# Performance work log

Measured on AMD Instinct MI355X. Metric: run time of the kernel, lower is better.

## Reference

```python
import jax, jax.numpy as jnp
import numpy as np

QDEPTH = 8
WIDTH = 64
HEIGHT = 64
WIRES = 12  # ceil(log2(64*64))
BATCH = 1024


def setup_inputs() -> dict:
    key = jax.random.key(0)
    k1, k2 = jax.random.split(key)
    x = jax.random.normal(k1, (BATCH, 1, WIDTH, HEIGHT), dtype=jnp.float32)
    # torch.nn.Parameter(torch.randn(weight_shape) * 0.4)
    weights = jax.random.normal(k2, (QDEPTH, WIRES, 3), dtype=jnp.float32) * 0.4
    return {"x": x, "weights": weights, "reps": 1}


def _rot_matrices(angles):
    # angles: (L, W, 3) -> (L, W, 2, 2) complex64; Rot(phi, theta, omega) = RZ(omega) RY(theta) RZ(phi)
    phi, theta, omega = angles[..., 0], angles[..., 1], angles[..., 2]
    c = jnp.cos(theta * 0.5).astype(jnp.complex64)
    s = jnp.sin(theta * 0.5).astype(jnp.complex64)
    ep = jnp.exp(-0.5j * (phi + omega).astype(jnp.complex64))  # e^{-i(phi+omega)/2}
    em = jnp.exp(-0.5j * (phi - omega).astype(jnp.complex64))  # e^{-i(phi-omega)/2}
    row0 = jnp.stack([ep * c, -jnp.conj(em) * s], axis=-1)
    row1 = jnp.stack([em * s, jnp.conj(ep) * c], axis=-1)
    return jnp.stack([row0, row1], axis=-2)


def _apply_1q(state, U, wire):
    # state: (B, 2, 2, ..., 2); apply 2x2 U on axis wire+1
    ax = wire + 1
    s = jnp.moveaxis(state, ax, -1)
    s = s @ U.T  # out[..., i] = sum_j U[i, j] s[..., j]
    return jnp.moveaxis(s, -1, ax)


def _apply_cnot(state, control, target):
    c, t = control + 1, target + 1
    s0, s1 = jnp.split(state, 2, axis=c)   # control = 0 / 1 halves
    s1 = jnp.flip(s1, axis=t)              # X on target where control = 1
    return jnp.concatenate([s0, s1], axis=c)


def _sel_layer(state, mats_l, r):
    # one StronglyEntanglingLayers layer: Rot on every wire, then CNOT ring of range r
    for w in range(WIRES):
        state = _apply_1q(state, mats_l[w], w)
    for w in range(WIRES):
        state = _apply_cnot(state, w, (w + r) % WIRES)
    return state


def _circuit(state, weights, reps):
    mats = _rot_matrices(jnp.tanh(weights))  # qw_map.tanh applied to raw weights
    for _ in range(reps):
        for l in range(QDEPTH):
            r = (l % (WIRES - 1)) + 1  # PennyLane default ranges
            layer = jax.checkpoint(lambda s, m, _r=r: _sel_layer(s, m, _r))
            state = layer(state, mats[l])
    return state


def reference(x, weights, reps):
    b = x.shape[0]
    v = x.reshape(b, -1)  # (b, 4096)
    norm = jnp.linalg.norm(v, axis=-1, keepdims=True)
    v = (v / norm).astype(jnp.complex64)
    state = v.reshape((b,) + (2,) * WIRES)
    state = _circuit(state, weights, reps)
    out = state.reshape(b, -1) * norm
    return out.reshape(b, 1, WIDTH, HEIGHT)
```

## Files before the change

kernel.cpp:

```cpp
#include <hip/hip_runtime.h>

#define WIRES   12
#define NSTATE  4096
#define QDEPTH  8
#define BLOCK   256
#define PER_T   16

using f2 = __attribute__((ext_vector_type(2))) float;

__device__ __forceinline__ int slotf(int a) { return a + (a >> 4); }

constexpr int colF(int l, int j) {
    int rr = (l % (WIRES - 1)) + 1;
    int v = 1 << j;
    for (int k = WIRES - 1; k >= 0; --k) {
        int bc = 11 - k;
        int bt = 11 - ((k + rr) % WIRES);
        v ^= ((v >> bc) & 1) << bt;
    }
    return v;
}
struct ColsT { int v[QDEPTH][WIRES]; };
constexpr ColsT mkCols() {
    ColsT c{};
    for (int l = 0; l < QDEPTH; ++l)
        for (int j = 0; j < WIRES; ++j) c.v[l][j] = colF(l, j);
    return c;
}
static __device__ const ColsT COLS = mkCols();

__global__ void mats_kernel(const float* __restrict__ wts, f2* __restrict__ mg)
{
    int t = blockIdx.x * blockDim.x + threadIdx.x;
    if (t >= QDEPTH * WIRES) return;
    float phi   = tanhf(wts[t * 3 + 0]);
    float theta = tanhf(wts[t * 3 + 1]);
    float omega = tanhf(wts[t * 3 + 2]);
    float c  = cosf(theta * 0.5f);
    float s  = sinf(theta * 0.5f);
    float a  = 0.5f * (phi + omega);
    float bm = 0.5f * (phi - omega);
    float ca = cosf(a),  sa = sinf(a);
    float cb = cosf(bm), sb = sinf(bm);
    f2* m = mg + t * 8;
    m[0] = f2{ c * ca,  c * ca};
    m[1] = f2{ c * sa, -c * sa};
    m[2] = f2{-s * cb, -s * cb};
    m[3] = f2{ s * sb, -s * sb};
    m[4] = f2{ s * cb,  s * cb};
    m[5] = f2{ s * sb, -s * sb};
    m[6] = f2{ c * ca,  c * ca};
    m[7] = f2{-c * sa,  c * sa};
}

template<int P>
__device__ __forceinline__ void gate(f2 r[PER_T], const f2* __restrict__ m)
{
    const f2 u00r = m[0], u00w = m[1], u01r = m[2], u01w = m[3];
    const f2 u10r = m[4], u10w = m[5], u11r = m[6], u11w = m[7];
    #pragma unroll
    for (int pr = 0; pr < PER_T / 2; pr += 2) {
        const int k0 = ((pr >> P) << (P + 1)) | (pr & ((1 << P) - 1));
        const int k1 = k0 | (1 << P);
        const int q  = pr + 1;
        const int j0 = ((q >> P) << (P + 1)) | (q & ((1 << P) - 1));
        const int j1 = j0 | (1 << P);
        f2 a0, b0, a1, b1;
        asm("v_pk_mul_f32 %0, %4, %8\n\t"
            "v_pk_mul_f32 %1, %4, %12\n\t"
            "v_pk_mul_f32 %2, %6, %8\n\t"
            "v_pk_mul_f32 %3, %6, %12\n\t"
            "v_pk_fma_f32 %0, %4, %9, %0 op_sel:[1,0,0] op_sel_hi:[0,1,1]\n\t"
            "v_pk_fma_f32 %1, %4, %13, %1 op_sel:[1,0,0] op_sel_hi:[0,1,1]\n\t"
            "v_pk_fma_f32 %2, %6, %9, %2 op_sel:[1,0,0] op_sel_hi:[0,1,1]\n\t"
            "v_pk_fma_f32 %3, %6, %13, %3 op_sel:[1,0,0] op_sel_hi:[0,1,1]\n\t"
            "v_pk_fma_f32 %0, %5, %10, %0\n\t"
            "v_pk_fma_f32 %1, %5, %14, %1\n\t"
            "v_pk_fma_f32 %2, %7, %10, %2\n\t"
            "v_pk_fma_f32 %3, %7, %14, %3\n\t"
            "v_pk_fma_f32 %0, %5, %11, %0 op_sel:[1,0,0] op_sel_hi:[0,1,1]\n\t"
            "v_pk_fma_f32 %1, %5, %15, %1 op_sel:[1,0,0] op_sel_hi:[0,1,1]\n\t"
            "v_pk_fma_f32 %2, %7, %11, %2 op_sel:[1,0,0] op_sel_hi:[0,1,1]\n\t"
            "v_pk_fma_f32 %3, %7, %15, %3 op_sel:[1,0,0] op_sel_hi:[0,1,1]"
            : "=&v"(a0), "=&v"(b0), "=&v"(a1), "=&v"(b1)
            : "v"(r[k0]), "v"(r[k1]), "v"(r[j0]), "v"(r[j1]),
              "v"(u00r), "v"(u00w), "v"(u01r), "v"(u01w),
              "v"(u10r), "v"(u10w), "v"(u11r), "v"(u11w));
        r[k0] = a0; r[k1] = b0; r[j0] = a1; r[j1] = b1;
    }
}

__global__ __launch_bounds__(BLOCK, 4) void qsim_kernel(
    const float* __restrict__ x,
    const f2*    __restrict__ mats_g,
    const int*   __restrict__ reps_ptr,
    float*       __restrict__ out,
    int write_mode)
{
    __shared__ f2 st[4352];

    const int g   = threadIdx.x;
    const int b   = blockIdx.x;
    const int ghi = g >> 4, glo = g & 15;
    const int w1b = 17 * g;
    const int rb1 = 272 * ghi + glo;
    const int rb2 = 17 * ghi + glo;

    const float4* xb4 = (const float4*)(x + (size_t)b * NSTATE) + g * 4;
    f2 r[PER_T];
    #pragma unroll
    for (int c = 0; c < 4; ++c) {
        float4 v = xb4[c];
        r[4*c+0] = f2{v.x, 0.f};
        r[4*c+1] = f2{v.y, 0.f};
        r[4*c+2] = f2{v.z, 0.f};
        r[4*c+3] = f2{v.w, 0.f};
    }

    const int reps = reps_ptr[0];
    for (int rep = 0; rep < reps; ++rep) {
        #pragma unroll 1
        for (int l = 0; l < QDEPTH; ++l) {
            const f2* M = mats_g + l * WIRES * 8;

            gate<3>(r, M + 8*8);  gate<2>(r, M + 9*8);
            gate<1>(r, M + 10*8); gate<0>(r, M + 11*8);

            #pragma unroll
            for (int k = 0; k < PER_T; ++k) st[w1b + k] = r[k];
            __syncthreads();
            #pragma unroll
            for (int k = 0; k < PER_T; ++k) r[k] = st[rb1 + 17 * k];

            gate<3>(r, M + 4*8); gate<2>(r, M + 5*8);
            gate<1>(r, M + 6*8); gate<0>(r, M + 7*8);

            #pragma unroll
            for (int k = 0; k < PER_T; ++k) st[rb1 + 17 * k] = r[k];
            __syncthreads();
            #pragma unroll
            for (int k = 0; k < PER_T; ++k) r[k] = st[rb2 + 272 * k];

            gate<3>(r, M + 0*8); gate<2>(r, M + 1*8);
            gate<1>(r, M + 2*8); gate<0>(r, M + 3*8);

            #pragma unroll
            for (int k = 0; k < PER_T; ++k) st[rb2 + 272 * k] = r[k];
            __syncthreads();

            int Fg = 0;
            #pragma unroll
            for (int j = 0; j < 8; ++j)
                Fg ^= ((g >> j) & 1) ? COLS.v[l][4 + j] : 0;
            const int c0 = COLS.v[l][0], c1 = COLS.v[l][1];
            const int c2 = COLS.v[l][2], c3 = COLS.v[l][3];
            #pragma unroll
            for (int k = 0; k < PER_T; ++k) {
                int ck = ((k & 1) ? c0 : 0) ^ ((k & 2) ? c1 : 0) ^
                         ((k & 4) ? c2 : 0) ^ ((k & 8) ? c3 : 0);
                r[k] = st[slotf(Fg ^ ck)];
            }
            __syncthreads();
        }
    }

    if (write_mode == 0) {
        float4* ob4 = (float4*)(out + (size_t)b * NSTATE) + g * 4;
        #pragma unroll
        for (int c = 0; c < 4; ++c)
            ob4[c] = make_float4(r[4*c].x, r[4*c+1].x, r[4*c+2].x, r[4*c+3].x);
    } else {
        float4* ob4 = (float4*)((float2*)out + (size_t)b * NSTATE) + g * 8;
        #pragma unroll
        for (int k = 0; k < PER_T; k += 2)
            ob4[k >> 1] = make_float4(r[k].x, r[k].y, r[k+1].x, r[k+1].y);
    }
}

extern "C" void kernel_launch(void* const* d_in, const int* in_sizes, int n_in,
                              void* d_out, int out_size, void* d_ws, size_t ws_size,
                              hipStream_t stream) {
    const float* x    = (const float*)d_in[0];
    const float* wts  = (const float*)d_in[1];
    const int*   reps = (const int*)d_in[2];
    float*       out  = (float*)d_out;
    f2*          mg   = (f2*)d_ws;
    (void)in_sizes; (void)n_in; (void)ws_size;

    const int write_mode = (out_size >= 2 * 1024 * NSTATE) ? 1 : 0;

    mats_kernel<<<1, 128, 0, stream>>>(wts, mg);
    qsim_kernel<<<1024, BLOCK, 0, stream>>>(x, mg, reps, out, write_mode);
}
```

Before: 145.6 us.

## Use 512 threads with 8 amplitudes each and four 3-qubit gate passes

Each block now has 512 threads, each holding 8 complex amplitudes instead of 16. Every layer is restructured into four passes of three in-register gates, where it used to be three passes of four, with new padded shared-memory index patterns for each transpose. This halves per-thread register pressure and allows higher occupancy. The cost is one extra shared-memory round trip and one extra barrier per layer.

```diff
diff --git a/kernel.cpp b/kernel.cpp
--- a/kernel.cpp
+++ b/kernel.cpp
@@ -3,8 +3,8 @@
 #define WIRES   12
 #define NSTATE  4096
 #define QDEPTH  8
-#define BLOCK   256
-#define PER_T   16
+#define BLOCK   512
+#define PER_T   8
 
 using f2 = __attribute__((ext_vector_type(2))) float;
 
@@ -90,7 +90,7 @@
     }
 }
 
-__global__ __launch_bounds__(BLOCK, 4) void qsim_kernel(
+__global__ __launch_bounds__(BLOCK, 8) void qsim_kernel(
     const float* __restrict__ x,
     const f2*    __restrict__ mats_g,
     const int*   __restrict__ reps_ptr,
@@ -101,15 +101,16 @@
 
     const int g   = threadIdx.x;
     const int b   = blockIdx.x;
-    const int ghi = g >> 4, glo = g & 15;
-    const int w1b = 17 * g;
-    const int rb1 = 272 * ghi + glo;
-    const int rb2 = 17 * ghi + glo;
+    const int m3  = (g >> 3) & 7;
+    const int w1b = 8 * g + (g >> 1);
+    const int r1b = 68 * (g >> 3) + (g & 7);
+    const int r2b = 544 * (g >> 6) + 8 * m3 + (m3 >> 1) + (g & 7);
+    const int r3b = g + (g >> 4);
 
-    const float4* xb4 = (const float4*)(x + (size_t)b * NSTATE) + g * 4;
+    const float4* xb4 = (const float4*)(x + (size_t)b * NSTATE) + g * 2;
     f2 r[PER_T];
     #pragma unroll
-    for (int c = 0; c < 4; ++c) {
+    for (int c = 0; c < 2; ++c) {
         float4 v = xb4[c];
         r[4*c+0] = f2{v.x, 0.f};
         r[4*c+1] = f2{v.y, 0.f};
@@ -123,41 +124,45 @@
         for (int l = 0; l < QDEPTH; ++l) {
             const f2* M = mats_g + l * WIRES * 8;
 
-            gate<3>(r, M + 8*8);  gate<2>(r, M + 9*8);
-            gate<1>(r, M + 10*8); gate<0>(r, M + 11*8);
+            gate<2>(r, M + 9*8); gate<1>(r, M + 10*8); gate<0>(r, M + 11*8);
 
             #pragma unroll
             for (int k = 0; k < PER_T; ++k) st[w1b + k] = r[k];
             __syncthreads();
             #pragma unroll
-            for (int k = 0; k < PER_T; ++k) r[k] = st[rb1 + 17 * k];
+            for (int k = 0; k < PER_T; ++k) r[k] = st[r1b + 8*k + (k >> 1)];
 
-            gate<3>(r, M + 4*8); gate<2>(r, M + 5*8);
-            gate<1>(r, M + 6*8); gate<0>(r, M + 7*8);
+            gate<2>(r, M + 6*8); gate<1>(r, M + 7*8); gate<0>(r, M + 8*8);
 
             #pragma unroll
-            for (int k = 0; k < PER_T; ++k) st[rb1 + 17 * k] = r[k];
+            for (int k = 0; k < PER_T; ++k) st[r1b + 8*k + (k >> 1)] = r[k];
             __syncthreads();
             #pragma unroll
-            for (int k = 0; k < PER_T; ++k) r[k] = st[rb2 + 272 * k];
+            for (int k = 0; k < PER_T; ++k) r[k] = st[r2b + 68*k];
 
-            gate<3>(r, M + 0*8); gate<2>(r, M + 1*8);
-            gate<1>(r, M + 2*8); gate<0>(r, M + 3*8);
+            gate<2>(r, M + 3*8); gate<1>(r, M + 4*8); gate<0>(r, M + 5*8);
 
             #pragma unroll
-            for (int k = 0; k < PER_T; ++k) st[rb2 + 272 * k] = r[k];
+            for (int k = 0; k < PER_T; ++k) st[r2b + 68*k] = r[k];
+            __syncthreads();
+            #pragma unroll
+            for (int k = 0; k < PER_T; ++k) r[k] = st[r3b + 544*k];
+
+            gate<2>(r, M + 0*8); gate<1>(r, M + 1*8); gate<0>(r, M + 2*8);
+
+            #pragma unroll
+            for (int k = 0; k < PER_T; ++k) st[r3b + 544*k] = r[k];
             __syncthreads();
 
             int Fg = 0;
             #pragma unroll
-            for (int j = 0; j < 8; ++j)
-                Fg ^= ((g >> j) & 1) ? COLS.v[l][4 + j] : 0;
-            const int c0 = COLS.v[l][0], c1 = COLS.v[l][1];
-            const int c2 = COLS.v[l][2], c3 = COLS.v[l][3];
+            for (int j = 0; j < 9; ++j)
+                Fg ^= ((g >> j) & 1) ? COLS.v[l][3 + j] : 0;
+            const int c0 = COLS.v[l][0], c1 = COLS.v[l][1], c2 = COLS.v[l][2];
             #pragma unroll
             for (int k = 0; k < PER_T; ++k) {
                 int ck = ((k & 1) ? c0 : 0) ^ ((k & 2) ? c1 : 0) ^
-                         ((k & 4) ? c2 : 0) ^ ((k & 8) ? c3 : 0);
+                         ((k & 4) ? c2 : 0);
                 r[k] = st[slotf(Fg ^ ck)];
             }
             __syncthreads();
@@ -165,12 +170,12 @@
     }
 
     if (write_mode == 0) {
-        float4* ob4 = (float4*)(out + (size_t)b * NSTATE) + g * 4;
+        float4* ob4 = (float4*)(out + (size_t)b * NSTATE) + g * 2;
         #pragma unroll
-        for (int c = 0; c < 4; ++c)
+        for (int c = 0; c < 2; ++c)
             ob4[c] = make_float4(r[4*c].x, r[4*c+1].x, r[4*c+2].x, r[4*c+3].x);
     } else {
-        float4* ob4 = (float4*)((float2*)out + (size_t)b * NSTATE) + g * 8;
+        float4* ob4 = (float4*)((float2*)out + (size_t)b * NSTATE) + g * 4;
         #pragma unroll
         for (int k = 0; k < PER_T; k += 2)
             ob4[k >> 1] = make_float4(r[k].x, r[k].y, r[k+1].x, r[k+1].y);
```

Result: slower. 151.3 us (+3.9%).

## Process two batch elements per block to halve barriers and share gate matrices

Applied to the files above, without the earlier changes.

Each block now simulates two state vectors with interleaved register sets and two shared-memory buffers, and the grid shrinks to 512 blocks. Barriers and gate-matrix loads are shared across both states, which gives the scheduler independent work to overlap with LDS latency. The cost is doubled registers and LDS per block, lowered launch-bounds occupancy, and only 512 blocks for 256 CUs, so load balance may suffer.

```diff
diff --git a/kernel.cpp b/kernel.cpp
--- a/kernel.cpp
+++ b/kernel.cpp
@@ -90,31 +90,36 @@
     }
 }
 
-__global__ __launch_bounds__(BLOCK, 4) void qsim_kernel(
+__global__ __launch_bounds__(BLOCK, 2) void qsim_kernel(
     const float* __restrict__ x,
     const f2*    __restrict__ mats_g,
     const int*   __restrict__ reps_ptr,
     float*       __restrict__ out,
     int write_mode)
 {
-    __shared__ f2 st[4352];
+    __shared__ f2 st[2 * 4352];
+    f2* const sA = st;
+    f2* const sB = st + 4352;
 
     const int g   = threadIdx.x;
-    const int b   = blockIdx.x;
+    const int eA  = blockIdx.x * 2;
+    const int eB  = eA + 1;
     const int ghi = g >> 4, glo = g & 15;
     const int w1b = 17 * g;
     const int rb1 = 272 * ghi + glo;
     const int rb2 = 17 * ghi + glo;
 
-    const float4* xb4 = (const float4*)(x + (size_t)b * NSTATE) + g * 4;
-    f2 r[PER_T];
+    const float4* xA4 = (const float4*)(x + (size_t)eA * NSTATE) + g * 4;
+    const float4* xB4 = (const float4*)(x + (size_t)eB * NSTATE) + g * 4;
+    f2 rA[PER_T], rB[PER_T];
     #pragma unroll
     for (int c = 0; c < 4; ++c) {
-        float4 v = xb4[c];
-        r[4*c+0] = f2{v.x, 0.f};
-        r[4*c+1] = f2{v.y, 0.f};
-        r[4*c+2] = f2{v.z, 0.f};
-        r[4*c+3] = f2{v.w, 0.f};
+        float4 va = xA4[c];
+        rA[4*c+0] = f2{va.x, 0.f}; rA[4*c+1] = f2{va.y, 0.f};
+        rA[4*c+2] = f2{va.z, 0.f}; rA[4*c+3] = f2{va.w, 0.f};
+        float4 vb = xB4[c];
+        rB[4*c+0] = f2{vb.x, 0.f}; rB[4*c+1] = f2{vb.y, 0.f};
+        rB[4*c+2] = f2{vb.z, 0.f}; rB[4*c+3] = f2{vb.w, 0.f};
     }
 
     const int reps = reps_ptr[0];
@@ -123,29 +128,44 @@
         for (int l = 0; l < QDEPTH; ++l) {
             const f2* M = mats_g + l * WIRES * 8;
 
-            gate<3>(r, M + 8*8);  gate<2>(r, M + 9*8);
-            gate<1>(r, M + 10*8); gate<0>(r, M + 11*8);
-
-            #pragma unroll
-            for (int k = 0; k < PER_T; ++k) st[w1b + k] = r[k];
-            __syncthreads();
-            #pragma unroll
-            for (int k = 0; k < PER_T; ++k) r[k] = st[rb1 + 17 * k];
-
-            gate<3>(r, M + 4*8); gate<2>(r, M + 5*8);
-            gate<1>(r, M + 6*8); gate<0>(r, M + 7*8);
-
-            #pragma unroll
-            for (int k = 0; k < PER_T; ++k) st[rb1 + 17 * k] = r[k];
-            __syncthreads();
-            #pragma unroll
-            for (int k = 0; k < PER_T; ++k) r[k] = st[rb2 + 272 * k];
-
-            gate<3>(r, M + 0*8); gate<2>(r, M + 1*8);
-            gate<1>(r, M + 2*8); gate<0>(r, M + 3*8);
-
-            #pragma unroll
-            for (int k = 0; k < PER_T; ++k) st[rb2 + 272 * k] = r[k];
+            gate<3>(rA, M + 8*8);  gate<2>(rA, M + 9*8);
+            gate<1>(rA, M + 10*8); gate<0>(rA, M + 11*8);
+            #pragma unroll
+            for (int k = 0; k < PER_T; ++k) sA[w1b + k] = rA[k];
+            gate<3>(rB, M + 8*8);  gate<2>(rB, M + 9*8);
+            gate<1>(rB, M + 10*8); gate<0>(rB, M + 11*8);
+            #pragma unroll
+            for (int k = 0; k < PER_T; ++k) sB[w1b + k] = rB[k];
+            __syncthreads();
+
+            #pragma unroll
+            for (int k = 0; k < PER_T; ++k) rA[k] = sA[rb1 + 17 * k];
+            #pragma unroll
+            for (int k = 0; k < PER_T; ++k) rB[k] = sB[rb1 + 17 * k];
+
+            gate<3>(rA, M + 4*8); gate<2>(rA, M + 5*8);
+            gate<1>(rA, M + 6*8); gate<0>(rA, M + 7*8);
+            #pragma unroll
+            for (int k = 0; k < PER_T; ++k) sA[rb1 + 17 * k] = rA[k];
+            gate<3>(rB, M + 4*8); gate<2>(rB, M + 5*8);
+            gate<1>(rB, M + 6*8); gate<0>(rB, M + 7*8);
+            #pragma unroll
+            for (int k = 0; k < PER_T; ++k) sB[rb1 + 17 * k] = rB[k];
+            __syncthreads();
+
+            #pragma unroll
+            for (int k = 0; k < PER_T; ++k) rA[k] = sA[rb2 + 272 * k];
+            #pragma unroll
+            for (int k = 0; k < PER_T; ++k) rB[k] = sB[rb2 + 272 * k];
+
+            gate<3>(rA, M + 0*8); gate<2>(rA, M + 1*8);
+            gate<1>(rA, M + 2*8); gate<0>(rA, M + 3*8);
+            #pragma unroll
+            for (int k = 0; k < PER_T; ++k) sA[rb2 + 272 * k] = rA[k];
+            gate<3>(rB, M + 0*8); gate<2>(rB, M + 1*8);
+            gate<1>(rB, M + 2*8); gate<0>(rB, M + 3*8);
+            #pragma unroll
+            for (int k = 0; k < PER_T; ++k) sB[rb2 + 272 * k] = rB[k];
             __syncthreads();
 
             int Fg = 0;
@@ -158,22 +178,30 @@
             for (int k = 0; k < PER_T; ++k) {
                 int ck = ((k & 1) ? c0 : 0) ^ ((k & 2) ? c1 : 0) ^
                          ((k & 4) ? c2 : 0) ^ ((k & 8) ? c3 : 0);
-                r[k] = st[slotf(Fg ^ ck)];
+                int s  = slotf(Fg ^ ck);
+                rA[k] = sA[s];
+                rB[k] = sB[s];
             }
             __syncthreads();
         }
     }
 
     if (write_mode == 0) {
-        float4* ob4 = (float4*)(out + (size_t)b * NSTATE) + g * 4;
+        float4* oA4 = (float4*)(out + (size_t)eA * NSTATE) + g * 4;
+        float4* oB4 = (float4*)(out + (size_t)eB * NSTATE) + g * 4;
         #pragma unroll
-        for (int c = 0; c < 4; ++c)
-            ob4[c] = make_float4(r[4*c].x, r[4*c+1].x, r[4*c+2].x, r[4*c+3].x);
+        for (int c = 0; c < 4; ++c) {
+            oA4[c] = make_float4(rA[4*c].x, rA[4*c+1].x, rA[4*c+2].x, rA[4*c+3].x);
+            oB4[c] = make_float4(rB[4*c].x, rB[4*c+1].x, rB[4*c+2].x, rB[4*c+3].x);
+        }
     } else {
-        float4* ob4 = (float4*)((float2*)out + (size_t)b * NSTATE) + g * 8;
+        float4* oA4 = (float4*)((float2*)out + (size_t)eA * NSTATE) + g * 8;
+        float4* oB4 = (float4*)((float2*)out + (size_t)eB * NSTATE) + g * 8;
         #pragma unroll
-        for (int k = 0; k < PER_T; k += 2)
-            ob4[k >> 1] = make_float4(r[k].x, r[k].y, r[k+1].x, r[k+1].y);
+        for (int k = 0; k < PER_T; k += 2) {
+            oA4[k >> 1] = make_float4(rA[k].x, rA[k].y, rA[k+1].x, rA[k+1].y);
+            oB4[k >> 1] = make_float4(rB[k].x, rB[k].y, rB[k+1].x, rB[k+1].y);
+        }
     }
 }
 
@@ -190,5 +218,5 @@
     const int write_mode = (out_size >= 2 * 1024 * NSTATE) ? 1 : 0;
 
     mats_kernel<<<1, 128, 0, stream>>>(wts, mg);
-    qsim_kernel<<<1024, BLOCK, 0, stream>>>(x, mg, reps, out, write_mode);
-}
+    qsim_kernel<<<512, BLOCK, 0, stream>>>(x, mg, reps, out, write_mode);
+}
```

After: 151.0 us. 1.04x slower.

## Use DPP cross-lane gates and XOR-swizzled LDS to drop one shuffle pass

Applied to the files above, without the earlier changes.

Two of the twelve single-qubit gates per stage now run across adjacent lanes with DPP quad permutes (0xB1, 0x4E) instead of in registers. Each stage therefore covers six wires instead of four, so one LDS transpose round trip and its barrier per layer go away. The shared buffer loses its padding and uses an XOR swizzle (sig) for bank-conflict avoidance, and the CNOT permutation read is remapped to match. In exchange, each DPP gate adds lane moves and duplicated arithmetic, and the new index mappings must stay consistent for the result to be correct.

```diff
diff --git a/kernel.cpp b/kernel.cpp
--- a/kernel.cpp
+++ b/kernel.cpp
@@ -8,7 +8,8 @@
 
 using f2 = __attribute__((ext_vector_type(2))) float;
 
-__device__ __forceinline__ int slotf(int a) { return a + (a >> 4); }
+__device__ __forceinline__ int sig(int a) { return a ^ ((a >> 4) & 15) ^ ((a >> 8) & 15); }
+constexpr int ck1(int k) { return (k << 6) ^ ((k & 3) << 2) ^ (k >> 2); }
 
 constexpr int colF(int l, int j) {
     int rr = (l % (WIRES - 1)) + 1;
@@ -90,6 +91,54 @@
     }
 }
 
+template<int CTRL>
+__device__ __forceinline__ f2 dpp_xor(f2 v) {
+    f2 o;
+    o.x = __int_as_float(__builtin_amdgcn_update_dpp(
+            0, __float_as_int(v.x), CTRL, 0xF, 0xF, true));
+    o.y = __int_as_float(__builtin_amdgcn_update_dpp(
+            0, __float_as_int(v.y), CTRL, 0xF, 0xF, true));
+    return o;
+}
+
+template<int CTRL>
+__device__ __forceinline__ void dppgate(f2 r[PER_T], const f2* __restrict__ m, bool hb)
+{
+    const f2 usr = hb ? m[6] : m[0];
+    const f2 usw = hb ? m[7] : m[1];
+    const f2 uor = hb ? m[4] : m[2];
+    const f2 uow = hb ? m[5] : m[3];
+    #pragma unroll
+    for (int k0 = 0; k0 < PER_T; k0 += 4) {
+        f2 p0 = dpp_xor<CTRL>(r[k0 + 0]);
+        f2 p1 = dpp_xor<CTRL>(r[k0 + 1]);
+        f2 p2 = dpp_xor<CTRL>(r[k0 + 2]);
+        f2 p3 = dpp_xor<CTRL>(r[k0 + 3]);
+        f2 a0, a1, a2, a3;
+        asm("v_pk_mul_f32 %0, %4, %12\n\t"
+            "v_pk_mul_f32 %1, %5, %12\n\t"
+            "v_pk_mul_f32 %2, %6, %12\n\t"
+            "v_pk_mul_f32 %3, %7, %12\n\t"
+            "v_pk_fma_f32 %0, %4, %13, %0 op_sel:[1,0,0] op_sel_hi:[0,1,1]\n\t"
+            "v_pk_fma_f32 %1, %5, %13, %1 op_sel:[1,0,0] op_sel_hi:[0,1,1]\n\t"
+            "v_pk_fma_f32 %2, %6, %13, %2 op_sel:[1,0,0] op_sel_hi:[0,1,1]\n\t"
+            "v_pk_fma_f32 %3, %7, %13, %3 op_sel:[1,0,0] op_sel_hi:[0,1,1]\n\t"
+            "v_pk_fma_f32 %0, %8, %14, %0\n\t"
+            "v_pk_fma_f32 %1, %9, %14, %1\n\t"
+            "v_pk_fma_f32 %2, %10, %14, %2\n\t"
+            "v_pk_fma_f32 %3, %11, %14, %3\n\t"
+            "v_pk_fma_f32 %0, %8, %15, %0 op_sel:[1,0,0] op_sel_hi:[0,1,1]\n\t"
+            "v_pk_fma_f32 %1, %9, %15, %1 op_sel:[1,0,0] op_sel_hi:[0,1,1]\n\t"
+            "v_pk_fma_f32 %2, %10, %15, %2 op_sel:[1,0,0] op_sel_hi:[0,1,1]\n\t"
+            "v_pk_fma_f32 %3, %11, %15, %3 op_sel:[1,0,0] op_sel_hi:[0,1,1]"
+            : "=&v"(a0), "=&v"(a1), "=&v"(a2), "=&v"(a3)
+            : "v"(r[k0]), "v"(r[k0 + 1]), "v"(r[k0 + 2]), "v"(r[k0 + 3]),
+              "v"(p0), "v"(p1), "v"(p2), "v"(p3),
+              "v"(usr), "v"(usw), "v"(uor), "v"(uow));
+        r[k0] = a0; r[k0 + 1] = a1; r[k0 + 2] = a2; r[k0 + 3] = a3;
+    }
+}
+
 __global__ __launch_bounds__(BLOCK, 4) void qsim_kernel(
     const float* __restrict__ x,
     const f2*    __restrict__ mats_g,
@@ -97,14 +146,17 @@
     float*       __restrict__ out,
     int write_mode)
 {
-    __shared__ f2 st[4352];
-
-    const int g   = threadIdx.x;
-    const int b   = blockIdx.x;
-    const int ghi = g >> 4, glo = g & 15;
-    const int w1b = 17 * g;
-    const int rb1 = 272 * ghi + glo;
-    const int rb2 = 17 * ghi + glo;
+    __shared__ f2 st[4096];
+
+    const int g  = threadIdx.x;
+    const int b  = blockIdx.x;
+    const bool hb0 = (g & 1) != 0;
+    const bool hb1 = (g & 2) != 0;
+
+    const int hg  = (g ^ (g >> 4)) & 15;
+    const int w1b = g << 4;
+    const int A   = ((g >> 2) & 15) | (((g >> 6) & 3) << 4) | ((g & 3) << 10);
+    const int r1b = sig(A);
 
     const float4* xb4 = (const float4*)(x + (size_t)b * NSTATE) + g * 4;
     f2 r[PER_T];
@@ -123,42 +175,38 @@
         for (int l = 0; l < QDEPTH; ++l) {
             const f2* M = mats_g + l * WIRES * 8;
 
-            gate<3>(r, M + 8*8);  gate<2>(r, M + 9*8);
-            gate<1>(r, M + 10*8); gate<0>(r, M + 11*8);
-
-            #pragma unroll
-            for (int k = 0; k < PER_T; ++k) st[w1b + k] = r[k];
+            gate<0>(r, M + 11*8); gate<1>(r, M + 10*8);
+            gate<2>(r, M + 9*8);  gate<3>(r, M + 8*8);
+            dppgate<0xB1>(r, M + 7*8, hb0);
+            dppgate<0x4E>(r, M + 6*8, hb1);
+
+            #pragma unroll
+            for (int k = 0; k < PER_T; ++k) st[w1b + (hg ^ k)] = r[k];
             __syncthreads();
             #pragma unroll
-            for (int k = 0; k < PER_T; ++k) r[k] = st[rb1 + 17 * k];
-
-            gate<3>(r, M + 4*8); gate<2>(r, M + 5*8);
-            gate<1>(r, M + 6*8); gate<0>(r, M + 7*8);
-
-            #pragma unroll
-            for (int k = 0; k < PER_T; ++k) st[rb1 + 17 * k] = r[k];
+            for (int k = 0; k < PER_T; ++k) r[k] = st[r1b ^ ck1(k)];
+
+            gate<0>(r, M + 5*8); gate<1>(r, M + 4*8);
+            gate<2>(r, M + 3*8); gate<3>(r, M + 2*8);
+            dppgate<0xB1>(r, M + 1*8, hb0);
+            dppgate<0x4E>(r, M + 0*8, hb1);
+
+            #pragma unroll
+            for (int k = 0; k < PER_T; ++k) st[r1b ^ ck1(k)] = r[k];
             __syncthreads();
-            #pragma unroll
-            for (int k = 0; k < PER_T; ++k) r[k] = st[rb2 + 272 * k];
-
-            gate<3>(r, M + 0*8); gate<2>(r, M + 1*8);
-            gate<1>(r, M + 2*8); gate<0>(r, M + 3*8);
-
-            #pragma unroll
-            for (int k = 0; k < PER_T; ++k) st[rb2 + 272 * k] = r[k];
-            __syncthreads();
-
-            int Fg = 0;
+
+            int FA = 0;
             #pragma unroll
             for (int j = 0; j < 8; ++j)
-                Fg ^= ((g >> j) & 1) ? COLS.v[l][4 + j] : 0;
-            const int c0 = COLS.v[l][0], c1 = COLS.v[l][1];
-            const int c2 = COLS.v[l][2], c3 = COLS.v[l][3];
+                FA ^= ((g >> j) & 1) ? COLS.v[l][4 + j] : 0;
+            const int fb = sig(FA);
+            const int t0 = sig(COLS.v[l][0]), t1 = sig(COLS.v[l][1]);
+            const int t2 = sig(COLS.v[l][2]), t3 = sig(COLS.v[l][3]);
             #pragma unroll
             for (int k = 0; k < PER_T; ++k) {
-                int ck = ((k & 1) ? c0 : 0) ^ ((k & 2) ? c1 : 0) ^
-                         ((k & 4) ? c2 : 0) ^ ((k & 8) ? c3 : 0);
-                r[k] = st[slotf(Fg ^ ck)];
+                int ct = ((k & 1) ? t0 : 0) ^ ((k & 2) ? t1 : 0) ^
+                         ((k & 4) ? t2 : 0) ^ ((k & 8) ? t3 : 0);
+                r[k] = st[fb ^ ct];
             }
             __syncthreads();
         }
```

Result: slower. 154.1 us (+5.8%).
